# Performance work log

Hardware: AMD Instinct MI355X
Metric: run time of the kernel (lower is better)

The kernel has to match this reference:

```python
import jax, jax.numpy as jnp
import numpy as np

R_MAX = 5.0
AVG_NEI = 16.0
NB = 8
L_OF_LM = np.repeat(np.arange(4), [1, 3, 5, 7])  # lm index -> l, 16 components for l_max=3


def real_sph(u):
    # real spherical harmonics up to l=3, component normalization; u: [E,3] unit vectors
    x, y, z = u[:, 0], u[:, 1], u[:, 2]
    x2, y2, z2 = x * x, y * y, z * z
    return jnp.stack([
        jnp.ones_like(x),
        1.7320508 * x, 1.7320508 * y, 1.7320508 * z,
        3.8729833 * x * y, 3.8729833 * y * z,
        1.1180340 * (3.0 * z2 - 1.0),
        3.8729833 * x * z, 1.9364917 * (x2 - y2),
        2.0916500 * y * (3.0 * x2 - y2), 10.246951 * x * y * z,
        1.6201852 * y * (5.0 * z2 - 1.0), 1.3228757 * z * (5.0 * z2 - 3.0),
        1.6201852 * x * (5.0 * z2 - 1.0), 5.1234753 * z * (x2 - y2),
        2.0916500 * x * (x2 - 3.0 * y2),
    ], axis=-1)


def radial_embed(r):
    # Bessel basis * polynomial (p=5) envelope, as in MACE RadialEmbeddingBlock
    n = jnp.arange(1, NB + 1, dtype=r.dtype)
    bess = jnp.sqrt(2.0 / R_MAX) * jnp.sin(n * jnp.pi * r[:, None] / R_MAX) / (r[:, None] + 1e-8)
    p = 5.0
    t = jnp.clip(r / R_MAX, 0.0, 1.0)
    env = 1.0 - 0.5 * (p + 1) * (p + 2) * t**p + p * (p + 2) * t**(p + 1) - 0.5 * p * (p + 1) * t**(p + 2)
    return bess * env[:, None]


def interaction(feats, Y, R, senders, receivers, Wu, Wd, num_nodes):
    # feats: [N,C,Din] (Din = sum of (2l+1) over input l-blocks); Y: [E,16]; R: [E,C,12] radial path weights
    n_lin = Wu.shape[0]
    up = jnp.concatenate([
        jnp.einsum('ncm,cd->ndm', feats[:, :, l * l:(l + 1) * (l + 1)], Wu[l])
        for l in range(n_lin)], axis=-1)
    hs = up[senders]  # gather sender features [E,C,Din]
    R0, R1, R2 = R[..., 0:4], R[..., 4:8], R[..., 8:12]
    # CG path (0, l_sh) -> l_sh : scalar feature times Y_l
    msg = R0[:, :, L_OF_LM] * hs[:, :, 0:1] * Y[:, None, :]  # [E,C,16]
    for l in range(1, n_lin):
        sl = slice(l * l, (l + 1) * (l + 1))
        # CG path (l, 0) -> l
        msg = msg.at[:, :, sl].add(R1[:, :, l:l + 1] * hs[:, :, sl] * Y[:, None, 0:1])
        # CG path (l, l) -> 0 : invariant dot product
        msg = msg.at[:, :, 0].add(R2[:, :, l] * jnp.sum(hs[:, :, sl] * Y[:, None, sl], axis=-1))
    agg = jnp.zeros((num_nodes, msg.shape[1], msg.shape[2]), msg.dtype).at[receivers].add(msg) / AVG_NEI
    return jnp.einsum('ncm,mcd->ndm', agg, Wd[L_OF_LM])  # per-l linear down


def setup_inputs() -> dict:
    key = jax.random.key(0)
    ks = jax.random.split(key, 18)
    N, E, C, S = 10000, 160000, 64, 10
    f32 = jnp.float32
    rn = lambda k, shape, scale: jax.random.normal(k, shape, f32) * scale
    return {
        'edge_vectors': rn(ks[0], (E, 3), 1.5),
        'node_embed': rn(ks[1], (S, C), 0.3),
        'rw1': rn(ks[2], (2, NB, 64), 1.0 / np.sqrt(NB)),
        'rw2': rn(ks[3], (2, 64, C * 12), 1.0 / np.sqrt(64)),
        'lu0': rn(ks[4], (1, C, C), 1.0 / np.sqrt(C)),
        'lu1': rn(ks[5], (2, C, C), 1.0 / np.sqrt(C)),
        'ld': rn(ks[6], (2, 4, C, C), 1.0 / np.sqrt(C)),
        'sel_w': rn(ks[7], (S, 4, C, C), 1.0 / np.sqrt(C)),
        'prod_w0': rn(ks[8], (S, C, C), 1.0 / np.sqrt(C)),
        'prod_w1': rn(ks[9], (S, C, C), 1.0 / np.sqrt(C)),
        'res_w': rn(ks[10], (S, C, C), 1.0 / np.sqrt(C)),
        'read0': rn(ks[11], (C, 1), 1.0 / np.sqrt(C)),
        'mlp_w1': rn(ks[12], (C, 32), 1.0 / np.sqrt(C)),
        'mlp_w2': rn(ks[13], (32, 1), 1.0 / np.sqrt(32)),
        'node_species': jax.random.randint(ks[14], (N,), 0, S),
        'senders': jax.random.randint(ks[15], (E,), 0, N),
        'receivers': jax.random.randint(ks[16], (E,), 0, N),
    }


def reference(edge_vectors, node_embed, rw1, rw2, lu0, lu1, ld, sel_w, prod_w0,
              prod_w1, res_w, read0, mlp_w1, mlp_w2, node_species, senders, receivers):
    N = node_species.shape[0]
    C = node_embed.shape[1]
    r = jnp.linalg.norm(edge_vectors, axis=-1)
    u = edge_vectors / (r[:, None] + 1e-8)
    Y = real_sph(u)                      # [E,16]
    rb = radial_embed(r)                 # [E,8]
    R_all = [(jax.nn.silu(rb @ rw1[i]) @ rw2[i]).reshape(-1, C, 12) for i in range(2)]
    # ---- layer 0 (selector_tp, not last) ----
    f = node_embed[node_species][:, :, None]               # [N,C,1] scalar embed
    f = interaction(f, Y, R_all[0], senders, receivers, lu0, ld[0], N)  # [N,C,16]
    blocks = []
    for l in range(4):  # species-dependent selector TP (per-l channel mixing)
        sl = slice(l * l, (l + 1) * (l + 1))
        blocks.append(jnp.einsum('ncm,ncd->ndm', f[:, :, sl], sel_w[node_species, l]))
    f = jnp.concatenate(blocks, axis=-1)
    # product basis (correlation 3 polynomial in invariant channel), target C x (0e+1o)
    s = f[:, :, 0]
    f1 = jnp.einsum('ncm,ncd->ndm', f[:, :, :4] * (1.0 + s + s * s)[:, :, None], prod_w0[node_species])
    out0 = f1[:, :, 0] @ read0           # linear readout head  [N,1]
    # ---- layer 1 (last, residual) ----
    res = jnp.einsum('nc,ncd->nd', f1[:, :, 0], res_w[node_species])
    g = interaction(f1, Y, R_all[1], senders, receivers, lu1, ld[1], N)  # [N,C,16]
    inv = g[:, :, 0] + jnp.sum(g[:, :, 1:] ** 2, axis=-1)  # invariants from all l blocks
    f2 = jnp.einsum('nc,ncd->nd', inv + inv * inv, prod_w1[node_species]) + res
    out1 = jax.nn.silu(f2 @ mlp_w1) @ mlp_w2  # nonlinear readout  [N,1]
    # stack heads (axis=2) then layers (axis=1): [N, num_interactions, num_heads, 1]
    return jnp.stack([out0, out1], axis=1)[:, :, None, :]
```

## Files before the change

### kernel.cpp

```cpp
#include <hip/hip_runtime.h>
#include <math.h>


typedef _Float16 half8 __attribute__((ext_vector_type(8)));
typedef float f32x4 __attribute__((ext_vector_type(4)));

__device__ __forceinline__ float silu_f(float x) { return x / (1.0f + expf(-x)); }

__device__ __forceinline__ float reduce64(float v) {
#pragma unroll
  for (int off = 32; off > 0; off >>= 1) v += __shfl_xor(v, off, 64);
  return v;
}

__device__ __forceinline__ void compute_Y(float x, float y, float z, float* Y) {
  float x2 = x * x, y2 = y * y, z2 = z * z;
  Y[0] = 1.0f;
  Y[1] = 1.7320508f * x;
  Y[2] = 1.7320508f * y;
  Y[3] = 1.7320508f * z;
  Y[4] = 3.8729833f * x * y;
  Y[5] = 3.8729833f * y * z;
  Y[6] = 1.118034f * (3.0f * z2 - 1.0f);
  Y[7] = 3.8729833f * x * z;
  Y[8] = 1.9364917f * (x2 - y2);
  Y[9] = 2.09165f * y * (3.0f * x2 - y2);
  Y[10] = 10.246951f * x * y * z;
  Y[11] = 1.6201852f * y * (5.0f * z2 - 1.0f);
  Y[12] = 1.3228757f * z * (5.0f * z2 - 3.0f);
  Y[13] = 1.6201852f * x * (5.0f * z2 - 1.0f);
  Y[14] = 5.1234753f * z * (x2 - y2);
  Y[15] = 2.09165f * x * (x2 - 3.0f * y2);
}

__device__ __forceinline__ void compute_rb(float r, float inv_r, float* rb) {
  float t = fminf(r * 0.2f, 1.0f);
  float t2 = t * t;
  float t5 = t2 * t2 * t;
  float env = 1.0f + t5 * (-21.0f + t * (35.0f - 15.0f * t));
  float th = 0.62831853f * r;
  float s1 = sinf(th), c1 = cosf(th);
  float c2 = 2.0f * c1;
  float sprev = 0.0f, scur = s1;
  float coef = 0.63245553f * inv_r * env;
#pragma unroll
  for (int k = 0; k < 8; k++) {
    rb[k] = coef * scur;
    float snxt = c2 * scur - sprev;
    sprev = scur; scur = snxt;
  }
}

__global__ __launch_bounds__(256) void k_hist(const int* __restrict__ receivers,
                                              int* __restrict__ cnt, int E) {
  int e = blockIdx.x * 256 + threadIdx.x;
  if (e < E) atomicAdd(&cnt[receivers[e]], 1);
}

__global__ __launch_bounds__(256) void k_scan(const int* __restrict__ deg,
                                              int* __restrict__ row_start,
                                              int* __restrict__ cursor, int N) {
  __shared__ int part[256];
  int t = threadIdx.x;
  int K = (N + 255) / 256;
  int lo = t * K, hi = min(lo + K, N);
  int s = 0;
  for (int i = lo; i < hi; i++) s += deg[i];
  part[t] = s;
  __syncthreads();
  for (int d = 1; d < 256; d <<= 1) {
    int v = (t >= d) ? part[t - d] : 0;
    __syncthreads();
    part[t] += v;
    __syncthreads();
  }
  int run = (t == 0) ? 0 : part[t - 1];
  for (int i = lo; i < hi; i++) {
    int di = deg[i];
    row_start[i] = run;
    cursor[i] = run;
    run += di;
  }
  if (t == 255) row_start[N] = part[255];
}

__global__ __launch_bounds__(256) void k_scatter(const int* __restrict__ receivers,
                                                 const int* __restrict__ senders,
                                                 int* __restrict__ cursor,
                                                 int* __restrict__ perm,
                                                 int* __restrict__ rsort,
                                                 int* __restrict__ ssort, int E) {
  int e = blockIdx.x * 256 + threadIdx.x;
  if (e < E) {
    int r = receivers[e];
    int pos = atomicAdd(&cursor[r], 1);
    perm[pos] = e;
    rsort[pos] = r;
    ssort[pos] = senders[e];
  }
}

__global__ __launch_bounds__(256) void k_pack(const float* __restrict__ rw2,
                                              _Float16* __restrict__ b1t,
                                              _Float16* __restrict__ b2t) {
  int idx = blockIdx.x * 256 + threadIdx.x;
  if (idx < 16384) {
    int n = idx >> 6, k = idx & 63;
    int c = n >> 2, j = n & 3;
    b1t[idx] = (_Float16)rw2[k * 768 + c * 12 + j];
  } else if (idx < 40960) {
    int i2 = idx - 16384;
    int n = i2 >> 6, k = i2 & 63;
    int c = n / 6, j = n - c * 6;
    int col = (j < 4) ? j : ((j == 4) ? 5 : 9);
    b2t[i2] = (_Float16)rw2[49152 + k * 768 + c * 12 + col];
  }
}

__global__ __launch_bounds__(256) void k_up0(const float* __restrict__ embed,
                                             const float* __restrict__ lu0,
                                             const int* __restrict__ species,
                                             float* __restrict__ up0, int N) {
  int wave = threadIdx.x >> 6, lane = threadIdx.x & 63;
  int n = (blockIdx.x << 2) + wave;
  if (n >= N) return;
  int sp = species[n];
  const float* er = embed + sp * 64;
  float acc = 0.0f;
#pragma unroll 8
  for (int c = 0; c < 64; c++) acc += er[c] * lu0[c * 64 + lane];
  up0[(size_t)n * 64 + lane] = acc;
}

__global__ __launch_bounds__(256) void k_geom(const float* __restrict__ ev,
                                              const float* __restrict__ rw1,
                                              const int* __restrict__ perm,
                                              _Float16* __restrict__ hid0,
                                              _Float16* __restrict__ hid1,
                                              float* __restrict__ Ysort,
                                              int* __restrict__ rsort,
                                              int* __restrict__ ssort,
                                              int E, int EPAD) {
  int wave = threadIdx.x >> 6, lane = threadIdx.x & 63;
  int j = blockIdx.x * 4 + wave;
  if (j >= EPAD) return;
  if (j >= E) {
    hid0[(size_t)j * 64 + lane] = (_Float16)0.0f;
    hid1[(size_t)j * 64 + lane] = (_Float16)0.0f;
    if (lane == 0) { rsort[j] = -1; ssort[j] = 0; }
    if (lane < 16) Ysort[(size_t)j * 16 + lane] = 0.0f;
    return;
  }
  int e = perm[j];
  float vx = ev[e * 3 + 0], vy = ev[e * 3 + 1], vz = ev[e * 3 + 2];
  float r = sqrtf(vx * vx + vy * vy + vz * vz);
  float inv_r = 1.0f / (r + 1e-8f);
  float Y[16]; compute_Y(vx * inv_r, vy * inv_r, vz * inv_r, Y);
  float rb[8]; compute_rb(r, inv_r, rb);

  float h0 = 0.0f, h1 = 0.0f;
#pragma unroll
  for (int k = 0; k < 8; k++) {
    h0 += rb[k] * rw1[k * 64 + lane];
    h1 += rb[k] * rw1[512 + k * 64 + lane];
  }
  hid0[(size_t)j * 64 + lane] = (_Float16)silu_f(h0);
  hid1[(size_t)j * 64 + lane] = (_Float16)silu_f(h1);

  float yv = Y[0];
#pragma unroll
  for (int m = 1; m < 16; m++) yv = (lane == m) ? Y[m] : yv;
  if (lane < 16) Ysort[(size_t)j * 16 + lane] = yv;
}

__global__ __launch_bounds__(256) void k_fagg1(const _Float16* __restrict__ hid,
                                               const _Float16* __restrict__ bt,
                                               const float* __restrict__ Ysort,
                                               const float* __restrict__ up0,
                                               const int* __restrict__ ssort,
                                               const int* __restrict__ rsort,
                                               float* __restrict__ agg, int E) {
  __shared__ _Float16 __attribute__((aligned(16))) lds[4][16 * 256];
  int wave = threadIdx.x >> 6, lane = threadIdx.x & 63;
  int q = lane >> 4, mr = lane & 15;
  _Float16* L = lds[wave];
  int j0 = __builtin_amdgcn_readfirstlane((blockIdx.x * 4 + wave) * 16);

  int rs[16], ss[16];
#pragma unroll
  for (int t = 0; t < 16; t++) {
    rs[t] = rsort[j0 + t];
    ss[t] = ssort[j0 + t];
  }
  float hsv[16];
#pragma unroll
  for (int t = 0; t < 16; t++)
    hsv[t] = up0[((size_t)ss[t] << 6) + lane];

  const half8* Ap = (const half8*)(hid + (size_t)(j0 + mr) * 64 + q * 8);
  half8 a0 = Ap[0];
  half8 a1 = Ap[4];
  const _Float16* bp = bt + (size_t)mr * 64 + q * 8;
#pragma unroll
  for (int T = 0; T < 16; T++) {
    half8 b0 = *(const half8*)(bp + T * 1024);
    half8 b1 = *(const half8*)(bp + T * 1024 + 32);
    f32x4 acc = {0.f, 0.f, 0.f, 0.f};
    acc = __builtin_amdgcn_mfma_f32_16x16x32_f16(a0, b0, acc, 0, 0, 0);
    acc = __builtin_amdgcn_mfma_f32_16x16x32_f16(a1, b1, acc, 0, 0, 0);
#pragma unroll
    for (int r = 0; r < 4; r++)
      L[(q * 4 + r) * 256 + T * 16 + mr] = (_Float16)acc[r];
  }

  float accm[16];
#pragma unroll
  for (int m = 0; m < 16; m++) accm[m] = 0.0f;
  int cur_r = (j0 < E) ? rs[0] : -1;

#pragma unroll
  for (int t = 0; t < 16; t++) {
    int j = j0 + t;
    bool ok = (j < E);
    int rr = ok ? rs[t] : -2;
    if (rr != cur_r) {
      if (cur_r >= 0) {
        float* base = agg + ((size_t)cur_r << 10) + lane;
#pragma unroll
        for (int m = 0; m < 16; m++) atomicAdd(base + (m << 6), accm[m]);
      }
#pragma unroll
      for (int m = 0; m < 16; m++) accm[m] = 0.0f;
      cur_r = rr;
    }
    if (ok) {
      float hs0 = hsv[t];
      const _Float16* Rr = L + t * 256 + lane * 4;
      float p0 = (float)Rr[0] * hs0, p1 = (float)Rr[1] * hs0;
      float p2 = (float)Rr[2] * hs0, p3 = (float)Rr[3] * hs0;
      const float* Yj = Ysort + (size_t)j * 16;
      float4 Ya = *(const float4*)(Yj);
      float4 Yb = *(const float4*)(Yj + 4);
      float4 Yc = *(const float4*)(Yj + 8);
      float4 Yd = *(const float4*)(Yj + 12);
      accm[0] += p0;
      accm[1] += p1 * Ya.y;  accm[2] += p1 * Ya.z;  accm[3] += p1 * Ya.w;
      accm[4] += p2 * Yb.x;  accm[5] += p2 * Yb.y;  accm[6] += p2 * Yb.z;
      accm[7] += p2 * Yb.w;  accm[8] += p2 * Yc.x;
      accm[9]  += p3 * Yc.y; accm[10] += p3 * Yc.z; accm[11] += p3 * Yc.w;
      accm[12] += p3 * Yd.x; accm[13] += p3 * Yd.y; accm[14] += p3 * Yd.z;
      accm[15] += p3 * Yd.w;
    }
  }
  if (cur_r >= 0) {
    float* base = agg + ((size_t)cur_r << 10) + lane;
#pragma unroll
    for (int m = 0; m < 16; m++) atomicAdd(base + (m << 6), accm[m]);
  }
}

__global__ __launch_bounds__(256) void k_fagg2(const _Float16* __restrict__ hid,
                                               const _Float16* __restrict__ bt,
                                               const float* __restrict__ Ysort,
                                               const float* __restrict__ up1,
                                               const int* __restrict__ ssort,
                                               const int* __restrict__ rsort,
                                               float* __restrict__ agg, int E) {
  __shared__ _Float16 __attribute__((aligned(16))) lds[4][16 * 384];
  int wave = threadIdx.x >> 6, lane = threadIdx.x & 63;
  int q = lane >> 4, mr = lane & 15;
  _Float16* L = lds[wave];
  int j0 = __builtin_amdgcn_readfirstlane((blockIdx.x * 4 + wave) * 16);

  int rs[16], ss[16];
#pragma unroll
  for (int t = 0; t < 16; t++) {
    rs[t] = rsort[j0 + t];
    ss[t] = ssort[j0 + t];
  }
  float4 hA[8];
#pragma unroll
  for (int t = 0; t < 8; t++)
    hA[t] = *(const float4*)(up1 + ((size_t)ss[t] << 8) + lane * 4);

  const half8* Ap = (const half8*)(hid + (size_t)(j0 + mr) * 64 + q * 8);
  half8 a0 = Ap[0];
  half8 a1 = Ap[4];
  const _Float16* bp = bt + (size_t)mr * 64 + q * 8;
#pragma unroll
  for (int T = 0; T < 24; T++) {
    half8 b0 = *(const half8*)(bp + T * 1024);
    half8 b1 = *(const half8*)(bp + T * 1024 + 32);
    f32x4 acc = {0.f, 0.f, 0.f, 0.f};
    acc = __builtin_amdgcn_mfma_f32_16x16x32_f16(a0, b0, acc, 0, 0, 0);
    acc = __builtin_amdgcn_mfma_f32_16x16x32_f16(a1, b1, acc, 0, 0, 0);
#pragma unroll
    for (int r = 0; r < 4; r++)
      L[(q * 4 + r) * 384 + T * 16 + mr] = (_Float16)acc[r];
  }

  float4 hB[8];
#pragma unroll
  for (int t = 0; t < 8; t++)
    hB[t] = *(const float4*)(up1 + ((size_t)ss[8 + t] << 8) + lane * 4);

  float accm[16];
#pragma unroll
  for (int m = 0; m < 16; m++) accm[m] = 0.0f;
  int cur_r = (j0 < E) ? rs[0] : -1;

#pragma unroll
  for (int t = 0; t < 16; t++) {
    int j = j0 + t;
    bool ok = (j < E);
    int rr = ok ? rs[t] : -2;
    if (rr != cur_r) {
      if (cur_r >= 0) {
        float* base = agg + ((size_t)cur_r << 10) + lane;
#pragma unroll
        for (int m = 0; m < 16; m++) atomicAdd(base + (m << 6), accm[m]);
      }
#pragma unroll
      for (int m = 0; m < 16; m++) accm[m] = 0.0f;
      cur_r = rr;
    }
    if (ok) {
      float4 hs = (t < 8) ? hA[t & 7] : hB[t & 7];
      float hs0 = hs.x, hs1 = hs.y, hs2 = hs.z, hs3 = hs.w;
      const _Float16* Rr = L + t * 384 + lane * 6;
      float R0 = (float)Rr[0], R1v = (float)Rr[1];
      float R2v = (float)Rr[2], R3v = (float)Rr[3];
      float c5 = (float)Rr[4], c9 = (float)Rr[5];
      float q0 = R0 * hs0, q1 = R1v * hs0, q2 = R2v * hs0, q3 = R3v * hs0;
      const float* Yj = Ysort + (size_t)j * 16;
      float4 Ya = *(const float4*)(Yj);
      float4 Yb = *(const float4*)(Yj + 4);
      float4 Yc = *(const float4*)(Yj + 8);
      float4 Yd = *(const float4*)(Yj + 12);
      accm[0] += q0 + c9 * (hs1 * Ya.y + hs2 * Ya.z + hs3 * Ya.w);
      accm[1] += q1 * Ya.y + c5 * hs1;
      accm[2] += q1 * Ya.z + c5 * hs2;
      accm[3] += q1 * Ya.w + c5 * hs3;
      accm[4] += q2 * Yb.x;  accm[5] += q2 * Yb.y;  accm[6] += q2 * Yb.z;
      accm[7] += q2 * Yb.w;  accm[8] += q2 * Yc.x;
      accm[9]  += q3 * Yc.y; accm[10] += q3 * Yc.z; accm[11] += q3 * Yc.w;
      accm[12] += q3 * Yd.x; accm[13] += q3 * Yd.y; accm[14] += q3 * Yd.z;
      accm[15] += q3 * Yd.w;
    }
  }
  if (cur_r >= 0) {
    float* base = agg + ((size_t)cur_r << 10) + lane;
#pragma unroll
    for (int m = 0; m < 16; m++) atomicAdd(base + (m << 6), accm[m]);
  }
}

__global__ __launch_bounds__(64) void k_node1(float* __restrict__ agg0,
                                              const float* __restrict__ ld0,
                                              const float* __restrict__ sel_w,
                                              const float* __restrict__ pw0,
                                              const float* __restrict__ res_w,
                                              const float* __restrict__ lu1,
                                              const float* __restrict__ read0,
                                              const int* __restrict__ species,
                                              float* __restrict__ out,
                                              float* __restrict__ res,
                                              float* __restrict__ up1, int N) {
  int n = blockIdx.x, d = threadIdx.x;
  int sp = species[n];
  __shared__ float sA[1024], sB[1024];

  float* ag = agg0 + ((size_t)n << 10);
#pragma unroll
  for (int m = 0; m < 16; m++) {
    sA[m * 64 + d] = ag[m * 64 + d] * 0.0625f;
    ag[m * 64 + d] = 0.0f;
  }
  __syncthreads();

  float fr[16];
#pragma unroll
  for (int m = 0; m < 16; m++) fr[m] = 0.0f;
#pragma unroll
  for (int l = 0; l < 4; l++) {
    int m0 = l * l, m1 = (l + 1) * (l + 1);
    const float* W = ld0 + l * 4096 + d;
#pragma unroll 8
    for (int c = 0; c < 64; c++) {
      float w = W[c * 64];
      for (int m = m0; m < m1; m++) fr[m] += sA[m * 64 + c] * w;
    }
  }
#pragma unroll
  for (int m = 0; m < 16; m++) sB[m * 64 + d] = fr[m];
  __syncthreads();

  float f2r[16];
#pragma unroll
  for (int m = 0; m < 16; m++) f2r[m] = 0.0f;
#pragma unroll
  for (int l = 0; l < 4; l++) {
    int m0 = l * l, m1 = (l + 1) * (l + 1);
    const float* W = sel_w + ((size_t)(sp * 4 + l) << 12) + d;
#pragma unroll 8
    for (int c = 0; c < 64; c++) {
      float w = W[c * 64];
      for (int m = m0; m < m1; m++) f2r[m] += sB[m * 64 + c] * w;
    }
  }
  float s0 = f2r[0];
  float tt = 1.0f + s0 + s0 * s0;
#pragma unroll
  for (int m = 0; m < 4; m++) sA[m * 64 + d] = f2r[m] * tt;
  __syncthreads();

  float f1r[4] = {0.f, 0.f, 0.f, 0.f};
  {
    const float* W = pw0 + ((size_t)sp << 12) + d;
#pragma unroll 8
    for (int c = 0; c < 64; c++) {
      float w = W[c * 64];
#pragma unroll
      for (int m = 0; m < 4; m++) f1r[m] += sA[m * 64 + c] * w;
    }
  }
#pragma unroll
  for (int m = 0; m < 4; m++) sB[m * 64 + d] = f1r[m];
  __syncthreads();

  float v = reduce64(f1r[0] * read0[d]);
  if (d == 0) out[2 * n] = v;

  float u0, u1v, u2v, u3v;
  {
    const float* Wr = res_w + ((size_t)sp << 12) + d;
    const float* Wu = lu1 + d;
    float a = 0.0f, b = 0.0f;
#pragma unroll 8
    for (int c = 0; c < 64; c++) {
      float fv = sB[c];
      a += fv * Wr[c * 64];
      b += fv * Wu[c * 64];
    }
    res[(size_t)n * 64 + d] = a;
    u0 = b;
  }
  {
    const float* Wu = lu1 + 4096 + d;
    float a1 = 0.f, a2 = 0.f, a3 = 0.f;
#pragma unroll 8
    for (int c = 0; c < 64; c++) {
      float w = Wu[c * 64];
      a1 += sB[64 + c] * w;
      a2 += sB[128 + c] * w;
      a3 += sB[192 + c] * w;
    }
    u1v = a1; u2v = a2; u3v = a3;
  }
  float4 uu = {u0, u1v, u2v, u3v};
  *(float4*)(up1 + ((size_t)n << 8) + d * 4) = uu;
}

__global__ __launch_bounds__(64) void k_node2(const float* __restrict__ agg1,
                                              const float* __restrict__ ld1,
                                              const float* __restrict__ pw1,
                                              const float* __restrict__ res,
                                              const float* __restrict__ mlp_w1,
                                              const float* __restrict__ mlp_w2,
                                              const int* __restrict__ species,
                                              float* __restrict__ out, int N) {
  int n = blockIdx.x, d = threadIdx.x;
  int sp = species[n];
  __shared__ float sA[1024];

  const float* ag = agg1 + ((size_t)n << 10);
#pragma unroll
  for (int m = 0; m < 16; m++) sA[m * 64 + d] = ag[m * 64 + d] * 0.0625f;
  __syncthreads();

  float g[16];
#pragma unroll
  for (int m = 0; m < 16; m++) g[m] = 0.0f;
#pragma unroll
  for (int l = 0; l < 4; l++) {
    int m0 = l * l, m1 = (l + 1) * (l + 1);
    const float* W = ld1 + l * 4096 + d;
#pragma unroll 8
    for (int c = 0; c < 64; c++) {
      float w = W[c * 64];
      for (int m = m0; m < m1; m++) g[m] += sA[m * 64 + c] * w;
    }
  }
  float inv = g[0];
#pragma unroll
  for (int m = 1; m < 16; m++) inv += g[m] * g[m];
  float qv = inv + inv * inv;
  __syncthreads();
  sA[d] = qv;
  __syncthreads();

  float a = res[(size_t)n * 64 + d];
  {
    const float* W = pw1 + ((size_t)sp << 12) + d;
#pragma unroll 8
    for (int c = 0; c < 64; c++) a += sA[c] * W[c * 64];
  }
  sA[64 + d] = a;
  __syncthreads();

  float val = 0.0f;
  if (d < 32) {
    float h = 0.0f;
#pragma unroll 8
    for (int c = 0; c < 64; c++) h += sA[64 + c] * mlp_w1[c * 32 + d];
    val = silu_f(h) * mlp_w2[d];
  }
  val = reduce64(val);
  if (d == 0) out[2 * n + 1] = val;
}

extern "C" void kernel_launch(void* const* d_in, const int* in_sizes, int n_in,
                              void* d_out, int out_size, void* d_ws, size_t ws_size,
                              hipStream_t stream) {
  const float* ev      = (const float*)d_in[0];
  const float* embed   = (const float*)d_in[1];
  const float* rw1     = (const float*)d_in[2];
  const float* rw2     = (const float*)d_in[3];
  const float* lu0     = (const float*)d_in[4];
  const float* lu1     = (const float*)d_in[5];
  const float* ld      = (const float*)d_in[6];
  const float* sel_w   = (const float*)d_in[7];
  const float* pw0     = (const float*)d_in[8];
  const float* pw1     = (const float*)d_in[9];
  const float* res_w   = (const float*)d_in[10];
  const float* read0   = (const float*)d_in[11];
  const float* mlp_w1  = (const float*)d_in[12];
  const float* mlp_w2  = (const float*)d_in[13];
  const int* species   = (const int*)d_in[14];
  const int* senders   = (const int*)d_in[15];
  const int* receivers = (const int*)d_in[16];
  float* out = (float*)d_out;

  int N = in_sizes[14];
  int E = in_sizes[15];
  int EPAD = ((E + 63) / 64) * 64;

  float* ws = (float*)d_ws;
  size_t o = 0;
  float* agg  = ws + o;  o += (size_t)N * 1024;
  float* up0  = ws + o;  o += (size_t)N * 64;
  float* up1  = ws + o;  o += (size_t)N * 256;
  float* resb = ws + o;  o += (size_t)N * 64;
  _Float16* b1t  = (_Float16*)(ws + o); o += 8192;
  _Float16* b2t  = (_Float16*)(ws + o); o += 12288;
  _Float16* hid0 = (_Float16*)(ws + o); o += (size_t)EPAD * 32;
  _Float16* hid1 = (_Float16*)(ws + o); o += (size_t)EPAD * 32;
  float* Ysort = ws + o; o += (size_t)EPAD * 16;
  int* row_start = (int*)(ws + o); o += (size_t)N + 1;
  int* cursor    = (int*)(ws + o); o += (size_t)N;
  int* perm      = (int*)(ws + o); o += (size_t)E;
  int* rsort     = (int*)(ws + o); o += (size_t)EPAD;
  int* ssort     = (int*)(ws + o); o += (size_t)EPAD;

  hipMemsetAsync(agg, 0, (size_t)N * 1024 * sizeof(float), stream);
  hipMemsetAsync(cursor, 0, (size_t)N * sizeof(int), stream);

  k_hist<<<(E + 255) / 256, 256, 0, stream>>>(receivers, cursor, E);
  k_scan<<<1, 256, 0, stream>>>(cursor, row_start, cursor, N);
  k_scatter<<<(E + 255) / 256, 256, 0, stream>>>(receivers, senders, cursor,
                                                 perm, rsort, ssort, E);

  k_pack<<<160, 256, 0, stream>>>(rw2, b1t, b2t);
  k_up0<<<(N + 3) / 4, 256, 0, stream>>>(embed, lu0, species, up0, N);
  k_geom<<<EPAD / 4, 256, 0, stream>>>(ev, rw1, perm, hid0, hid1, Ysort,
                                       rsort, ssort, E, EPAD);

  int fblocks = EPAD / 64;
  k_fagg1<<<fblocks, 256, 0, stream>>>(hid0, b1t, Ysort, up0, ssort, rsort, agg, E);
  k_node1<<<N, 64, 0, stream>>>(agg, ld, sel_w, pw0, res_w, lu1, read0, species,
                                out, resb, up1, N);
  k_fagg2<<<fblocks, 256, 0, stream>>>(hid1, b2t, Ysort, up1, ssort, rsort, agg, E);
  k_node2<<<N, 64, 0, stream>>>(agg, ld + 16384, pw1, resb, mlp_w1, mlp_w2, species, out, N);
}
```

Measured before the change: 500.0 us.

## Sort nodes by species and process two same-species nodes per wave in node kernels

Adds a counting sort of nodes by species, padded to multiples of 8 per species, so each wave handles two nodes that share species-dependent weights. Each weight load from global memory is reused for two nodes. The node kernels now use 256-thread blocks with one wave per node pair, and an m-major shared layout with float4 reads. This is meant to halve weight traffic and cut block-launch overhead. In exchange it adds three small sort kernels and a memset, doubles register pressure, and assumes at most 10 species.

Result: slower. 615.5 us (+23.1%).

```diff
diff --git a/kernel.cpp b/kernel.cpp
--- a/kernel.cpp
+++ b/kernel.cpp
@@ -51,6 +51,21 @@
   }
 }
 
+__device__ __forceinline__ void fma16(float* fr, const float* Ab, int c,
+                                      float w0, float w1, float w2, float w3) {
+  float4 a0 = *(const float4*)(Ab + c * 16);
+  float4 a1 = *(const float4*)(Ab + c * 16 + 4);
+  float4 a2 = *(const float4*)(Ab + c * 16 + 8);
+  float4 a3 = *(const float4*)(Ab + c * 16 + 12);
+  fr[0] += a0.x * w0;
+  fr[1] += a0.y * w1;  fr[2] += a0.z * w1;  fr[3] += a0.w * w1;
+  fr[4] += a1.x * w2;  fr[5] += a1.y * w2;  fr[6] += a1.z * w2;
+  fr[7] += a1.w * w2;  fr[8] += a2.x * w2;
+  fr[9] += a2.y * w3;  fr[10] += a2.z * w3; fr[11] += a2.w * w3;
+  fr[12] += a3.x * w3; fr[13] += a3.y * w3; fr[14] += a3.z * w3;
+  fr[15] += a3.w * w3;
+}
+
 __global__ __launch_bounds__(256) void k_hist(const int* __restrict__ receivers,
                                               int* __restrict__ cnt, int E) {
   int e = blockIdx.x * 256 + threadIdx.x;
@@ -97,6 +112,32 @@
     perm[pos] = e;
     rsort[pos] = r;
     ssort[pos] = senders[e];
+  }
+}
+
+__global__ __launch_bounds__(256) void k_nhist(const int* __restrict__ species,
+                                               int* __restrict__ scnt, int N) {
+  int n = blockIdx.x * 256 + threadIdx.x;
+  if (n < N) atomicAdd(&scnt[species[n]], 1);
+}
+
+__global__ void k_nscan(int* __restrict__ scnt) {
+  int run = 0;
+#pragma unroll
+  for (int s = 0; s < 10; s++) {
+    int c = scnt[s];
+    scnt[s] = run;
+    run += ((c + 7) / 8) * 8;
+  }
+}
+
+__global__ __launch_bounds__(256) void k_nscatter(const int* __restrict__ species,
+                                                  int* __restrict__ scnt,
+                                                  int* __restrict__ nsort, int N) {
+  int n = blockIdx.x * 256 + threadIdx.x;
+  if (n < N) {
+    int pos = atomicAdd(&scnt[species[n]], 1);
+    nsort[pos] = n;
   }
 }
 
@@ -355,168 +396,226 @@
   }
 }
 
-__global__ __launch_bounds__(64) void k_node1(float* __restrict__ agg0,
-                                              const float* __restrict__ ld0,
-                                              const float* __restrict__ sel_w,
-                                              const float* __restrict__ pw0,
-                                              const float* __restrict__ res_w,
-                                              const float* __restrict__ lu1,
-                                              const float* __restrict__ read0,
-                                              const int* __restrict__ species,
-                                              float* __restrict__ out,
-                                              float* __restrict__ res,
-                                              float* __restrict__ up1, int N) {
-  int n = blockIdx.x, d = threadIdx.x;
-  int sp = species[n];
-  __shared__ float sA[1024], sB[1024];
-
-  float* ag = agg0 + ((size_t)n << 10);
-#pragma unroll
-  for (int m = 0; m < 16; m++) {
-    sA[m * 64 + d] = ag[m * 64 + d] * 0.0625f;
-    ag[m * 64 + d] = 0.0f;
-  }
-  __syncthreads();
-
-  float fr[16];
-#pragma unroll
-  for (int m = 0; m < 16; m++) fr[m] = 0.0f;
-#pragma unroll
-  for (int l = 0; l < 4; l++) {
-    int m0 = l * l, m1 = (l + 1) * (l + 1);
-    const float* W = ld0 + l * 4096 + d;
-#pragma unroll 8
+__global__ __launch_bounds__(256) void k_node1(float* __restrict__ agg0,
+                                               const float* __restrict__ ld0,
+                                               const float* __restrict__ sel_w,
+                                               const float* __restrict__ pw0,
+                                               const float* __restrict__ res_w,
+                                               const float* __restrict__ lu1,
+                                               const float* __restrict__ read0,
+                                               const int* __restrict__ species,
+                                               const int* __restrict__ nsort,
+                                               float* __restrict__ out,
+                                               float* __restrict__ res,
+                                               float* __restrict__ up1) {
+  __shared__ float __attribute__((aligned(16))) sm[4][2][2][1024];
+  int wave = threadIdx.x >> 6, d = threadIdx.x & 63;
+  int i0 = blockIdx.x * 8 + wave * 2;
+  int n0 = nsort[i0], n1 = nsort[i0 + 1];
+  if (n0 < 0) return;
+  bool ok1 = (n1 >= 0);
+  int nv1 = ok1 ? n1 : n0;
+  int sp = species[n0];
+  float* A0 = sm[wave][0][0]; float* B0 = sm[wave][0][1];
+  float* A1 = sm[wave][1][0]; float* B1 = sm[wave][1][1];
+
+  {
+    float* ag = agg0 + ((size_t)n0 << 10);
+    float v[16];
+#pragma unroll
+    for (int m = 0; m < 16; m++) {
+      v[m] = ag[(m << 6) + d] * 0.0625f;
+      ag[(m << 6) + d] = 0.0f;
+    }
+#pragma unroll
+    for (int g = 0; g < 4; g++)
+      *(float4*)(A0 + d * 16 + g * 4) = make_float4(v[g*4], v[g*4+1], v[g*4+2], v[g*4+3]);
+  }
+  {
+    float* ag = agg0 + ((size_t)nv1 << 10);
+    float v[16];
+#pragma unroll
+    for (int m = 0; m < 16; m++) {
+      v[m] = ag[(m << 6) + d] * 0.0625f;
+      if (ok1) ag[(m << 6) + d] = 0.0f;
+    }
+#pragma unroll
+    for (int g = 0; g < 4; g++)
+      *(float4*)(A1 + d * 16 + g * 4) = make_float4(v[g*4], v[g*4+1], v[g*4+2], v[g*4+3]);
+  }
+
+  float fr0[16], fr1[16];
+#pragma unroll
+  for (int m = 0; m < 16; m++) { fr0[m] = 0.0f; fr1[m] = 0.0f; }
+#pragma unroll 4
+  for (int c = 0; c < 64; c++) {
+    float w0 = ld0[c * 64 + d];
+    float w1 = ld0[4096 + c * 64 + d];
+    float w2 = ld0[8192 + c * 64 + d];
+    float w3 = ld0[12288 + c * 64 + d];
+    fma16(fr0, A0, c, w0, w1, w2, w3);
+    fma16(fr1, A1, c, w0, w1, w2, w3);
+  }
+#pragma unroll
+  for (int g = 0; g < 4; g++) {
+    *(float4*)(B0 + d * 16 + g * 4) = make_float4(fr0[g*4], fr0[g*4+1], fr0[g*4+2], fr0[g*4+3]);
+    *(float4*)(B1 + d * 16 + g * 4) = make_float4(fr1[g*4], fr1[g*4+1], fr1[g*4+2], fr1[g*4+3]);
+  }
+
+  float f20[16], f21[16];
+#pragma unroll
+  for (int m = 0; m < 16; m++) { f20[m] = 0.0f; f21[m] = 0.0f; }
+  const float* Ws = sel_w + ((size_t)(sp * 4) << 12);
+#pragma unroll 4
+  for (int c = 0; c < 64; c++) {
+    float w0 = Ws[c * 64 + d];
+    float w1 = Ws[4096 + c * 64 + d];
+    float w2 = Ws[8192 + c * 64 + d];
+    float w3 = Ws[12288 + c * 64 + d];
+    fma16(f20, B0, c, w0, w1, w2, w3);
+    fma16(f21, B1, c, w0, w1, w2, w3);
+  }
+  {
+    float s0 = f20[0], tt = 1.0f + s0 + s0 * s0;
+    *(float4*)(A0 + d * 16) = make_float4(f20[0]*tt, f20[1]*tt, f20[2]*tt, f20[3]*tt);
+    float s1 = f21[0], tu = 1.0f + s1 + s1 * s1;
+    *(float4*)(A1 + d * 16) = make_float4(f21[0]*tu, f21[1]*tu, f21[2]*tu, f21[3]*tu);
+  }
+
+  float f10[4] = {0.f, 0.f, 0.f, 0.f}, f11[4] = {0.f, 0.f, 0.f, 0.f};
+  const float* Wp = pw0 + ((size_t)sp << 12);
+#pragma unroll 4
+  for (int c = 0; c < 64; c++) {
+    float w = Wp[c * 64 + d];
+    float4 a0 = *(const float4*)(A0 + c * 16);
+    float4 a1 = *(const float4*)(A1 + c * 16);
+    f10[0] += a0.x * w; f10[1] += a0.y * w; f10[2] += a0.z * w; f10[3] += a0.w * w;
+    f11[0] += a1.x * w; f11[1] += a1.y * w; f11[2] += a1.z * w; f11[3] += a1.w * w;
+  }
+  *(float4*)(B0 + d * 16) = make_float4(f10[0], f10[1], f10[2], f10[3]);
+  *(float4*)(B1 + d * 16) = make_float4(f11[0], f11[1], f11[2], f11[3]);
+
+  float rd = read0[d];
+  float v0 = reduce64(f10[0] * rd);
+  float v1 = reduce64(f11[0] * rd);
+  if (d == 0) {
+    out[2 * n0] = v0;
+    if (ok1) out[2 * n1] = v1;
+  }
+
+  float r0 = 0.f, u00 = 0.f, u01 = 0.f, u02 = 0.f, u03 = 0.f;
+  float r1 = 0.f, u10 = 0.f, u11 = 0.f, u12 = 0.f, u13 = 0.f;
+  const float* Wr = res_w + ((size_t)sp << 12);
+#pragma unroll 4
+  for (int c = 0; c < 64; c++) {
+    float wr = Wr[c * 64 + d];
+    float wu0 = lu1[c * 64 + d];
+    float wu1 = lu1[4096 + c * 64 + d];
+    float4 a0 = *(const float4*)(B0 + c * 16);
+    float4 a1 = *(const float4*)(B1 + c * 16);
+    r0 += a0.x * wr;  u00 += a0.x * wu0;
+    u01 += a0.y * wu1; u02 += a0.z * wu1; u03 += a0.w * wu1;
+    r1 += a1.x * wr;  u10 += a1.x * wu0;
+    u11 += a1.y * wu1; u12 += a1.z * wu1; u13 += a1.w * wu1;
+  }
+  res[((size_t)n0 << 6) + d] = r0;
+  *(float4*)(up1 + ((size_t)n0 << 8) + d * 4) = make_float4(u00, u01, u02, u03);
+  if (ok1) {
+    res[((size_t)n1 << 6) + d] = r1;
+    *(float4*)(up1 + ((size_t)n1 << 8) + d * 4) = make_float4(u10, u11, u12, u13);
+  }
+}
+
+__global__ __launch_bounds__(256) void k_node2(const float* __restrict__ agg1,
+                                               const float* __restrict__ ld1,
+                                               const float* __restrict__ pw1,
+                                               const float* __restrict__ res,
+                                               const float* __restrict__ mlp_w1,
+                                               const float* __restrict__ mlp_w2,
+                                               const int* __restrict__ species,
+                                               const int* __restrict__ nsort,
+                                               float* __restrict__ out) {
+  __shared__ float __attribute__((aligned(16))) sm[4][2][1024];
+  __shared__ float sq[4][2][64];
+  __shared__ float sf[4][2][64];
+  int wave = threadIdx.x >> 6, d = threadIdx.x & 63;
+  int i0 = blockIdx.x * 8 + wave * 2;
+  int n0 = nsort[i0], n1 = nsort[i0 + 1];
+  if (n0 < 0) return;
+  bool ok1 = (n1 >= 0);
+  int nv1 = ok1 ? n1 : n0;
+  int sp = species[n0];
+  float* A0 = sm[wave][0];
+  float* A1 = sm[wave][1];
+
+  {
+    const float* ag = agg1 + ((size_t)n0 << 10);
+    float v[16];
+#pragma unroll
+    for (int m = 0; m < 16; m++) v[m] = ag[(m << 6) + d] * 0.0625f;
+#pragma unroll
+    for (int g = 0; g < 4; g++)
+      *(float4*)(A0 + d * 16 + g * 4) = make_float4(v[g*4], v[g*4+1], v[g*4+2], v[g*4+3]);
+  }
+  {
+    const float* ag = agg1 + ((size_t)nv1 << 10);
+    float v[16];
+#pragma unroll
+    for (int m = 0; m < 16; m++) v[m] = ag[(m << 6) + d] * 0.0625f;
+#pragma unroll
+    for (int g = 0; g < 4; g++)
+      *(float4*)(A1 + d * 16 + g * 4) = make_float4(v[g*4], v[g*4+1], v[g*4+2], v[g*4+3]);
+  }
+
+  float g0[16], g1[16];
+#pragma unroll
+  for (int m = 0; m < 16; m++) { g0[m] = 0.0f; g1[m] = 0.0f; }
+#pragma unroll 4
+  for (int c = 0; c < 64; c++) {
+    float w0 = ld1[c * 64 + d];
+    float w1 = ld1[4096 + c * 64 + d];
+    float w2 = ld1[8192 + c * 64 + d];
+    float w3 = ld1[12288 + c * 64 + d];
+    fma16(g0, A0, c, w0, w1, w2, w3);
+    fma16(g1, A1, c, w0, w1, w2, w3);
+  }
+  float inv0 = g0[0], inv1 = g1[0];
+#pragma unroll
+  for (int m = 1; m < 16; m++) { inv0 += g0[m] * g0[m]; inv1 += g1[m] * g1[m]; }
+  sq[wave][0][d] = inv0 + inv0 * inv0;
+  sq[wave][1][d] = inv1 + inv1 * inv1;
+
+  float a0 = res[((size_t)n0 << 6) + d];
+  float a1 = res[((size_t)nv1 << 6) + d];
+  const float* Wp = pw1 + ((size_t)sp << 12);
+#pragma unroll 4
+  for (int c = 0; c < 64; c++) {
+    float w = Wp[c * 64 + d];
+    a0 += sq[wave][0][c] * w;
+    a1 += sq[wave][1][c] * w;
+  }
+  sf[wave][0][d] = a0;
+  sf[wave][1][d] = a1;
+
+  float val0 = 0.0f, val1 = 0.0f;
+  if (d < 32) {
+    float h0 = 0.0f, h1 = 0.0f;
+#pragma unroll 4
     for (int c = 0; c < 64; c++) {
-      float w = W[c * 64];
-      for (int m = m0; m < m1; m++) fr[m] += sA[m * 64 + c] * w;
+      float w = mlp_w1[c * 32 + d];
+      h0 += sf[wave][0][c] * w;
+      h1 += sf[wave][1][c] * w;
     }
-  }
-#pragma unroll
-  for (int m = 0; m < 16; m++) sB[m * 64 + d] = fr[m];
-  __syncthreads();
-
-  float f2r[16];
-#pragma unroll
-  for (int m = 0; m < 16; m++) f2r[m] = 0.0f;
-#pragma unroll
-  for (int l = 0; l < 4; l++) {
-    int m0 = l * l, m1 = (l + 1) * (l + 1);
-    const float* W = sel_w + ((size_t)(sp * 4 + l) << 12) + d;
-#pragma unroll 8
-    for (int c = 0; c < 64; c++) {
-      float w = W[c * 64];
-      for (int m = m0; m < m1; m++) f2r[m] += sB[m * 64 + c] * w;
-    }
-  }
-  float s0 = f2r[0];
-  float tt = 1.0f + s0 + s0 * s0;
-#pragma unroll
-  for (int m = 0; m < 4; m++) sA[m * 64 + d] = f2r[m] * tt;
-  __syncthreads();
-
-  float f1r[4] = {0.f, 0.f, 0.f, 0.f};
-  {
-    const float* W = pw0 + ((size_t)sp << 12) + d;
-#pragma unroll 8
-    for (int c = 0; c < 64; c++) {
-      float w = W[c * 64];
-#pragma unroll
-      for (int m = 0; m < 4; m++) f1r[m] += sA[m * 64 + c] * w;
-    }
-  }
-#pragma unroll
-  for (int m = 0; m < 4; m++) sB[m * 64 + d] = f1r[m];
-  __syncthreads();
-
-  float v = reduce64(f1r[0] * read0[d]);
-  if (d == 0) out[2 * n] = v;
-
-  float u0, u1v, u2v, u3v;
-  {
-    const float* Wr = res_w + ((size_t)sp << 12) + d;
-    const float* Wu = lu1 + d;
-    float a = 0.0f, b = 0.0f;
-#pragma unroll 8
-    for (int c = 0; c < 64; c++) {
-      float fv = sB[c];
-      a += fv * Wr[c * 64];
-      b += fv * Wu[c * 64];
-    }
-    res[(size_t)n * 64 + d] = a;
-    u0 = b;
-  }
-  {
-    const float* Wu = lu1 + 4096 + d;
-    float a1 = 0.f, a2 = 0.f, a3 = 0.f;
-#pragma unroll 8
-    for (int c = 0; c < 64; c++) {
-      float w = Wu[c * 64];
-      a1 += sB[64 + c] * w;
-      a2 += sB[128 + c] * w;
-      a3 += sB[192 + c] * w;
-    }
-    u1v = a1; u2v = a2; u3v = a3;
-  }
-  float4 uu = {u0, u1v, u2v, u3v};
-  *(float4*)(up1 + ((size_t)n << 8) + d * 4) = uu;
-}
-
-__global__ __launch_bounds__(64) void k_node2(const float* __restrict__ agg1,
-                                              const float* __restrict__ ld1,
-                                              const float* __restrict__ pw1,
-                                              const float* __restrict__ res,
-                                              const float* __restrict__ mlp_w1,
-                                              const float* __restrict__ mlp_w2,
-                                              const int* __restrict__ species,
-                                              float* __restrict__ out, int N) {
-  int n = blockIdx.x, d = threadIdx.x;
-  int sp = species[n];
-  __shared__ float sA[1024];
-
-  const float* ag = agg1 + ((size_t)n << 10);
-#pragma unroll
-  for (int m = 0; m < 16; m++) sA[m * 64 + d] = ag[m * 64 + d] * 0.0625f;
-  __syncthreads();
-
-  float g[16];
-#pragma unroll
-  for (int m = 0; m < 16; m++) g[m] = 0.0f;
-#pragma unroll
-  for (int l = 0; l < 4; l++) {
-    int m0 = l * l, m1 = (l + 1) * (l + 1);
-    const float* W = ld1 + l * 4096 + d;
-#pragma unroll 8
-    for (int c = 0; c < 64; c++) {
-      float w = W[c * 64];
-      for (int m = m0; m < m1; m++) g[m] += sA[m * 64 + c] * w;
-    }
-  }
-  float inv = g[0];
-#pragma unroll
-  for (int m = 1; m < 16; m++) inv += g[m] * g[m];
-  float qv = inv + inv * inv;
-  __syncthreads();
-  sA[d] = qv;
-  __syncthreads();
-
-  float a = res[(size_t)n * 64 + d];
-  {
-    const float* W = pw1 + ((size_t)sp << 12) + d;
-#pragma unroll 8
-    for (int c = 0; c < 64; c++) a += sA[c] * W[c * 64];
-  }
-  sA[64 + d] = a;
-  __syncthreads();
-
-  float val = 0.0f;
-  if (d < 32) {
-    float h = 0.0f;
-#pragma unroll 8
-    for (int c = 0; c < 64; c++) h += sA[64 + c] * mlp_w1[c * 32 + d];
-    val = silu_f(h) * mlp_w2[d];
-  }
-  val = reduce64(val);
-  if (d == 0) out[2 * n + 1] = val;
+    float w2 = mlp_w2[d];
+    val0 = silu_f(h0) * w2;
+    val1 = silu_f(h1) * w2;
+  }
+  val0 = reduce64(val0);
+  val1 = reduce64(val1);
+  if (d == 0) {
+    out[2 * n0 + 1] = val0;
+    if (ok1) out[2 * n1 + 1] = val1;
+  }
 }
 
 extern "C" void kernel_launch(void* const* d_in, const int* in_sizes, int n_in,
@@ -544,6 +643,7 @@
   int N = in_sizes[14];
   int E = in_sizes[15];
   int EPAD = ((E + 63) / 64) * 64;
+  int NP = ((N + 70 + 7) / 8) * 8;
 
   float* ws = (float*)d_ws;
   size_t o = 0;
@@ -558,18 +658,25 @@
   float* Ysort = ws + o; o += (size_t)EPAD * 16;
   int* row_start = (int*)(ws + o); o += (size_t)N + 1;
   int* cursor    = (int*)(ws + o); o += (size_t)N;
+  int* scnt      = (int*)(ws + o); o += 16;
   int* perm      = (int*)(ws + o); o += (size_t)E;
   int* rsort     = (int*)(ws + o); o += (size_t)EPAD;
   int* ssort     = (int*)(ws + o); o += (size_t)EPAD;
+  int* nsort     = (int*)(ws + o); o += (size_t)NP;
 
   hipMemsetAsync(agg, 0, (size_t)N * 1024 * sizeof(float), stream);
-  hipMemsetAsync(cursor, 0, (size_t)N * sizeof(int), stream);
+  hipMemsetAsync(cursor, 0, ((size_t)N + 16) * sizeof(int), stream);
+  hipMemsetAsync(nsort, 0xFF, (size_t)NP * sizeof(int), stream);
 
   k_hist<<<(E + 255) / 256, 256, 0, stream>>>(receivers, cursor, E);
   k_scan<<<1, 256, 0, stream>>>(cursor, row_start, cursor, N);
   k_scatter<<<(E + 255) / 256, 256, 0, stream>>>(receivers, senders, cursor,
                                                  perm, rsort, ssort, E);
 
+  k_nhist<<<(N + 255) / 256, 256, 0, stream>>>(species, scnt, N);
+  k_nscan<<<1, 1, 0, stream>>>(scnt);
+  k_nscatter<<<(N + 255) / 256, 256, 0, stream>>>(species, scnt, nsort, N);
+
   k_pack<<<160, 256, 0, stream>>>(rw2, b1t, b2t);
   k_up0<<<(N + 3) / 4, 256, 0, stream>>>(embed, lu0, species, up0, N);
   k_geom<<<EPAD / 4, 256, 0, stream>>>(ev, rw1, perm, hid0, hid1, Ysort,
@@ -577,8 +684,9 @@
 
   int fblocks = EPAD / 64;
   k_fagg1<<<fblocks, 256, 0, stream>>>(hid0, b1t, Ysort, up0, ssort, rsort, agg, E);
-  k_node1<<<N, 64, 0, stream>>>(agg, ld, sel_w, pw0, res_w, lu1, read0, species,
-                                out, resb, up1, N);
+  k_node1<<<NP / 8, 256, 0, stream>>>(agg, ld, sel_w, pw0, res_w, lu1, read0,
+                                      species, nsort, out, resb, up1);
   k_fagg2<<<fblocks, 256, 0, stream>>>(hid1, b2t, Ysort, up1, ssort, rsort, agg, E);
-  k_node2<<<N, 64, 0, stream>>>(agg, ld + 16384, pw1, resb, mlp_w1, mlp_w2, species, out, N);
-}
+  k_node2<<<NP / 8, 256, 0, stream>>>(agg, ld + 16384, pw1, resb, mlp_w1, mlp_w2,
+                                      species, nsort, out);
+}
```

## Sort nodes by species and process two same-species nodes per block

Applied to the files above, without the earlier changes.

Adds a counting sort of nodes by species, padding each species bucket to an even count with -1 sentinels. The node kernels then handle a pair of same-species nodes per 64-thread block, so each species-dependent and shared weight load from global memory feeds two nodes instead of one. This roughly halves weight traffic in the node stages. In exchange it doubles register and shared-memory use per block and adds three small launches plus a memset. The scnt buffer is placed right after cursor, and the memset is widened to clear it as well.

Result: slower. 675.3 us (+35.0%).

```diff
diff --git a/kernel.cpp b/kernel.cpp
--- a/kernel.cpp
+++ b/kernel.cpp
@@ -97,6 +97,32 @@
     perm[pos] = e;
     rsort[pos] = r;
     ssort[pos] = senders[e];
+  }
+}
+
+__global__ __launch_bounds__(256) void k_nhist(const int* __restrict__ species,
+                                               int* __restrict__ scnt, int N) {
+  int n = blockIdx.x * 256 + threadIdx.x;
+  if (n < N) atomicAdd(&scnt[species[n]], 1);
+}
+
+__global__ void k_nscan(int* __restrict__ scnt) {
+  int run = 0;
+#pragma unroll
+  for (int s = 0; s < 10; s++) {
+    int c = scnt[s];
+    scnt[s] = run;
+    run += ((c + 1) / 2) * 2;
+  }
+}
+
+__global__ __launch_bounds__(256) void k_nscatter(const int* __restrict__ species,
+                                                  int* __restrict__ scnt,
+                                                  int* __restrict__ nsort, int N) {
+  int n = blockIdx.x * 256 + threadIdx.x;
+  if (n < N) {
+    int pos = atomicAdd(&scnt[species[n]], 1);
+    nsort[pos] = n;
   }
 }
 
@@ -363,24 +389,38 @@
                                               const float* __restrict__ lu1,
                                               const float* __restrict__ read0,
                                               const int* __restrict__ species,
+                                              const int* __restrict__ nsort,
                                               float* __restrict__ out,
                                               float* __restrict__ res,
-                                              float* __restrict__ up1, int N) {
-  int n = blockIdx.x, d = threadIdx.x;
-  int sp = species[n];
-  __shared__ float sA[1024], sB[1024];
-
-  float* ag = agg0 + ((size_t)n << 10);
-#pragma unroll
-  for (int m = 0; m < 16; m++) {
-    sA[m * 64 + d] = ag[m * 64 + d] * 0.0625f;
-    ag[m * 64 + d] = 0.0f;
-  }
-  __syncthreads();
-
-  float fr[16];
-#pragma unroll
-  for (int m = 0; m < 16; m++) fr[m] = 0.0f;
+                                              float* __restrict__ up1) {
+  int d = threadIdx.x;
+  int i0 = blockIdx.x * 2;
+  int n0 = nsort[i0], n1 = nsort[i0 + 1];
+  if (n0 < 0) return;
+  bool ok1 = (n1 >= 0);
+  int nv1 = ok1 ? n1 : n0;
+  int sp = species[n0];
+  __shared__ float sA0[1024], sB0[1024], sA1[1024], sB1[1024];
+
+  {
+    float* ag = agg0 + ((size_t)n0 << 10);
+#pragma unroll
+    for (int m = 0; m < 16; m++) {
+      sA0[m * 64 + d] = ag[(m << 6) + d] * 0.0625f;
+      ag[(m << 6) + d] = 0.0f;
+    }
+    float* ag1 = agg0 + ((size_t)nv1 << 10);
+#pragma unroll
+    for (int m = 0; m < 16; m++) {
+      sA1[m * 64 + d] = ag1[(m << 6) + d] * 0.0625f;
+      if (ok1) ag1[(m << 6) + d] = 0.0f;
+    }
+  }
+  __syncthreads();
+
+  float fr0[16], fr1[16];
+#pragma unroll
+  for (int m = 0; m < 16; m++) { fr0[m] = 0.0f; fr1[m] = 0.0f; }
 #pragma unroll
   for (int l = 0; l < 4; l++) {
     int m0 = l * l, m1 = (l + 1) * (l + 1);
@@ -388,16 +428,19 @@
 #pragma unroll 8
     for (int c = 0; c < 64; c++) {
       float w = W[c * 64];
-      for (int m = m0; m < m1; m++) fr[m] += sA[m * 64 + c] * w;
-    }
-  }
-#pragma unroll
-  for (int m = 0; m < 16; m++) sB[m * 64 + d] = fr[m];
-  __syncthreads();
-
-  float f2r[16];
-#pragma unroll
-  for (int m = 0; m < 16; m++) f2r[m] = 0.0f;
+      for (int m = m0; m < m1; m++) {
+        fr0[m] += sA0[m * 64 + c] * w;
+        fr1[m] += sA1[m * 64 + c] * w;
+      }
+    }
+  }
+#pragma unroll
+  for (int m = 0; m < 16; m++) { sB0[m * 64 + d] = fr0[m]; sB1[m * 64 + d] = fr1[m]; }
+  __syncthreads();
+
+  float f20[16], f21[16];
+#pragma unroll
+  for (int m = 0; m < 16; m++) { f20[m] = 0.0f; f21[m] = 0.0f; }
 #pragma unroll
   for (int l = 0; l < 4; l++) {
     int m0 = l * l, m1 = (l + 1) * (l + 1);
@@ -405,60 +448,77 @@
 #pragma unroll 8
     for (int c = 0; c < 64; c++) {
       float w = W[c * 64];
-      for (int m = m0; m < m1; m++) f2r[m] += sB[m * 64 + c] * w;
-    }
-  }
-  float s0 = f2r[0];
-  float tt = 1.0f + s0 + s0 * s0;
-#pragma unroll
-  for (int m = 0; m < 4; m++) sA[m * 64 + d] = f2r[m] * tt;
-  __syncthreads();
-
-  float f1r[4] = {0.f, 0.f, 0.f, 0.f};
+      for (int m = m0; m < m1; m++) {
+        f20[m] += sB0[m * 64 + c] * w;
+        f21[m] += sB1[m * 64 + c] * w;
+      }
+    }
+  }
+  {
+    float s0 = f20[0], tt = 1.0f + s0 + s0 * s0;
+#pragma unroll
+    for (int m = 0; m < 4; m++) sA0[m * 64 + d] = f20[m] * tt;
+    float s1 = f21[0], tu = 1.0f + s1 + s1 * s1;
+#pragma unroll
+    for (int m = 0; m < 4; m++) sA1[m * 64 + d] = f21[m] * tu;
+  }
+  __syncthreads();
+
+  float f10[4] = {0.f, 0.f, 0.f, 0.f}, f11[4] = {0.f, 0.f, 0.f, 0.f};
   {
     const float* W = pw0 + ((size_t)sp << 12) + d;
 #pragma unroll 8
     for (int c = 0; c < 64; c++) {
       float w = W[c * 64];
 #pragma unroll
-      for (int m = 0; m < 4; m++) f1r[m] += sA[m * 64 + c] * w;
-    }
-  }
-#pragma unroll
-  for (int m = 0; m < 4; m++) sB[m * 64 + d] = f1r[m];
-  __syncthreads();
-
-  float v = reduce64(f1r[0] * read0[d]);
-  if (d == 0) out[2 * n] = v;
-
-  float u0, u1v, u2v, u3v;
+      for (int m = 0; m < 4; m++) {
+        f10[m] += sA0[m * 64 + c] * w;
+        f11[m] += sA1[m * 64 + c] * w;
+      }
+    }
+  }
+#pragma unroll
+  for (int m = 0; m < 4; m++) { sB0[m * 64 + d] = f10[m]; sB1[m * 64 + d] = f11[m]; }
+  __syncthreads();
+
+  float rd = read0[d];
+  float v0 = reduce64(f10[0] * rd);
+  float v1 = reduce64(f11[0] * rd);
+  if (d == 0) {
+    out[2 * n0] = v0;
+    if (ok1) out[2 * n1] = v1;
+  }
+
+  float u00, u10;
   {
     const float* Wr = res_w + ((size_t)sp << 12) + d;
     const float* Wu = lu1 + d;
-    float a = 0.0f, b = 0.0f;
-#pragma unroll 8
-    for (int c = 0; c < 64; c++) {
-      float fv = sB[c];
-      a += fv * Wr[c * 64];
-      b += fv * Wu[c * 64];
-    }
-    res[(size_t)n * 64 + d] = a;
-    u0 = b;
+    float a0 = 0.f, b0 = 0.f, a1 = 0.f, b1 = 0.f;
+#pragma unroll 8
+    for (int c = 0; c < 64; c++) {
+      float wr = Wr[c * 64], wu = Wu[c * 64];
+      float fv0 = sB0[c], fv1 = sB1[c];
+      a0 += fv0 * wr;  b0 += fv0 * wu;
+      a1 += fv1 * wr;  b1 += fv1 * wu;
+    }
+    res[((size_t)n0 << 6) + d] = a0;  u00 = b0;
+    if (ok1) res[((size_t)n1 << 6) + d] = a1;
+    u10 = b1;
   }
   {
     const float* Wu = lu1 + 4096 + d;
-    float a1 = 0.f, a2 = 0.f, a3 = 0.f;
+    float a01 = 0.f, a02 = 0.f, a03 = 0.f;
+    float a11 = 0.f, a12 = 0.f, a13 = 0.f;
 #pragma unroll 8
     for (int c = 0; c < 64; c++) {
       float w = Wu[c * 64];
-      a1 += sB[64 + c] * w;
-      a2 += sB[128 + c] * w;
-      a3 += sB[192 + c] * w;
-    }
-    u1v = a1; u2v = a2; u3v = a3;
-  }
-  float4 uu = {u0, u1v, u2v, u3v};
-  *(float4*)(up1 + ((size_t)n << 8) + d * 4) = uu;
+      a01 += sB0[64 + c] * w;  a02 += sB0[128 + c] * w;  a03 += sB0[192 + c] * w;
+      a11 += sB1[64 + c] * w;  a12 += sB1[128 + c] * w;  a13 += sB1[192 + c] * w;
+    }
+    *(float4*)(up1 + ((size_t)n0 << 8) + d * 4) = make_float4(u00, a01, a02, a03);
+    if (ok1)
+      *(float4*)(up1 + ((size_t)n1 << 8) + d * 4) = make_float4(u10, a11, a12, a13);
+  }
 }
 
 __global__ __launch_bounds__(64) void k_node2(const float* __restrict__ agg1,
@@ -468,19 +528,32 @@
                                               const float* __restrict__ mlp_w1,
                                               const float* __restrict__ mlp_w2,
                                               const int* __restrict__ species,
-                                              float* __restrict__ out, int N) {
-  int n = blockIdx.x, d = threadIdx.x;
-  int sp = species[n];
-  __shared__ float sA[1024];
-
-  const float* ag = agg1 + ((size_t)n << 10);
-#pragma unroll
-  for (int m = 0; m < 16; m++) sA[m * 64 + d] = ag[m * 64 + d] * 0.0625f;
-  __syncthreads();
-
-  float g[16];
-#pragma unroll
-  for (int m = 0; m < 16; m++) g[m] = 0.0f;
+                                              const int* __restrict__ nsort,
+                                              float* __restrict__ out) {
+  int d = threadIdx.x;
+  int i0 = blockIdx.x * 2;
+  int n0 = nsort[i0], n1 = nsort[i0 + 1];
+  if (n0 < 0) return;
+  bool ok1 = (n1 >= 0);
+  int nv1 = ok1 ? n1 : n0;
+  int sp = species[n0];
+  __shared__ float sA0[1024], sA1[1024];
+  __shared__ float sv0[128], sv1[128];
+
+  {
+    const float* ag = agg1 + ((size_t)n0 << 10);
+    const float* ag1 = agg1 + ((size_t)nv1 << 10);
+#pragma unroll
+    for (int m = 0; m < 16; m++) {
+      sA0[m * 64 + d] = ag[(m << 6) + d] * 0.0625f;
+      sA1[m * 64 + d] = ag1[(m << 6) + d] * 0.0625f;
+    }
+  }
+  __syncthreads();
+
+  float g0[16], g1[16];
+#pragma unroll
+  for (int m = 0; m < 16; m++) { g0[m] = 0.0f; g1[m] = 0.0f; }
 #pragma unroll
   for (int l = 0; l < 4; l++) {
     int m0 = l * l, m1 = (l + 1) * (l + 1);
@@ -488,35 +561,54 @@
 #pragma unroll 8
     for (int c = 0; c < 64; c++) {
       float w = W[c * 64];
-      for (int m = m0; m < m1; m++) g[m] += sA[m * 64 + c] * w;
-    }
-  }
-  float inv = g[0];
-#pragma unroll
-  for (int m = 1; m < 16; m++) inv += g[m] * g[m];
-  float qv = inv + inv * inv;
-  __syncthreads();
-  sA[d] = qv;
-  __syncthreads();
-
-  float a = res[(size_t)n * 64 + d];
+      for (int m = m0; m < m1; m++) {
+        g0[m] += sA0[m * 64 + c] * w;
+        g1[m] += sA1[m * 64 + c] * w;
+      }
+    }
+  }
+  float inv0 = g0[0], inv1 = g1[0];
+#pragma unroll
+  for (int m = 1; m < 16; m++) { inv0 += g0[m] * g0[m]; inv1 += g1[m] * g1[m]; }
+  __syncthreads();
+  sv0[d] = inv0 + inv0 * inv0;
+  sv1[d] = inv1 + inv1 * inv1;
+  __syncthreads();
+
+  float a0 = res[((size_t)n0 << 6) + d];
+  float a1 = res[((size_t)nv1 << 6) + d];
   {
     const float* W = pw1 + ((size_t)sp << 12) + d;
 #pragma unroll 8
-    for (int c = 0; c < 64; c++) a += sA[c] * W[c * 64];
-  }
-  sA[64 + d] = a;
-  __syncthreads();
-
-  float val = 0.0f;
+    for (int c = 0; c < 64; c++) {
+      float w = W[c * 64];
+      a0 += sv0[c] * w;
+      a1 += sv1[c] * w;
+    }
+  }
+  sv0[64 + d] = a0;
+  sv1[64 + d] = a1;
+  __syncthreads();
+
+  float val0 = 0.0f, val1 = 0.0f;
   if (d < 32) {
-    float h = 0.0f;
-#pragma unroll 8
-    for (int c = 0; c < 64; c++) h += sA[64 + c] * mlp_w1[c * 32 + d];
-    val = silu_f(h) * mlp_w2[d];
-  }
-  val = reduce64(val);
-  if (d == 0) out[2 * n + 1] = val;
+    float h0 = 0.0f, h1 = 0.0f;
+#pragma unroll 8
+    for (int c = 0; c < 64; c++) {
+      float w = mlp_w1[c * 32 + d];
+      h0 += sv0[64 + c] * w;
+      h1 += sv1[64 + c] * w;
+    }
+    float w2 = mlp_w2[d];
+    val0 = silu_f(h0) * w2;
+    val1 = silu_f(h1) * w2;
+  }
+  val0 = reduce64(val0);
+  val1 = reduce64(val1);
+  if (d == 0) {
+    out[2 * n0 + 1] = val0;
+    if (ok1) out[2 * n1 + 1] = val1;
+  }
 }
 
 extern "C" void kernel_launch(void* const* d_in, const int* in_sizes, int n_in,
@@ -544,6 +636,7 @@
   int N = in_sizes[14];
   int E = in_sizes[15];
   int EPAD = ((E + 63) / 64) * 64;
+  int NP = ((N + 10 * 2 + 1) / 2) * 2;
 
   float* ws = (float*)d_ws;
   size_t o = 0;
@@ -558,18 +651,25 @@
   float* Ysort = ws + o; o += (size_t)EPAD * 16;
   int* row_start = (int*)(ws + o); o += (size_t)N + 1;
   int* cursor    = (int*)(ws + o); o += (size_t)N;
+  int* scnt      = (int*)(ws + o); o += 16;
   int* perm      = (int*)(ws + o); o += (size_t)E;
   int* rsort     = (int*)(ws + o); o += (size_t)EPAD;
   int* ssort     = (int*)(ws + o); o += (size_t)EPAD;
+  int* nsort     = (int*)(ws + o); o += (size_t)NP;
 
   hipMemsetAsync(agg, 0, (size_t)N * 1024 * sizeof(float), stream);
-  hipMemsetAsync(cursor, 0, (size_t)N * sizeof(int), stream);
+  hipMemsetAsync(cursor, 0, ((size_t)N + 16) * sizeof(int), stream);
+  hipMemsetAsync(nsort, 0xFF, (size_t)NP * sizeof(int), stream);
 
   k_hist<<<(E + 255) / 256, 256, 0, stream>>>(receivers, cursor, E);
   k_scan<<<1, 256, 0, stream>>>(cursor, row_start, cursor, N);
   k_scatter<<<(E + 255) / 256, 256, 0, stream>>>(receivers, senders, cursor,
                                                  perm, rsort, ssort, E);
 
+  k_nhist<<<(N + 255) / 256, 256, 0, stream>>>(species, scnt, N);
+  k_nscan<<<1, 1, 0, stream>>>(scnt);
+  k_nscatter<<<(N + 255) / 256, 256, 0, stream>>>(species, scnt, nsort, N);
+
   k_pack<<<160, 256, 0, stream>>>(rw2, b1t, b2t);
   k_up0<<<(N + 3) / 4, 256, 0, stream>>>(embed, lu0, species, up0, N);
   k_geom<<<EPAD / 4, 256, 0, stream>>>(ev, rw1, perm, hid0, hid1, Ysort,
@@ -577,8 +677,9 @@
 
   int fblocks = EPAD / 64;
   k_fagg1<<<fblocks, 256, 0, stream>>>(hid0, b1t, Ysort, up0, ssort, rsort, agg, E);
-  k_node1<<<N, 64, 0, stream>>>(agg, ld, sel_w, pw0, res_w, lu1, read0, species,
-                                out, resb, up1, N);
+  k_node1<<<NP / 2, 64, 0, stream>>>(agg, ld, sel_w, pw0, res_w, lu1, read0,
+                                     species, nsort, out, resb, up1);
   k_fagg2<<<fblocks, 256, 0, stream>>>(hid1, b2t, Ysort, up1, ssort, rsort, agg, E);
-  k_node2<<<N, 64, 0, stream>>>(agg, ld + 16384, pw1, resb, mlp_w1, mlp_w2, species, out, N);
-}
+  k_node2<<<NP / 2, 64, 0, stream>>>(agg, ld + 16384, pw1, resb, mlp_w1, mlp_w2,
+                                     species, nsort, out);
+}
```
